# Kernel tuning notes

Hardware: AMD Instinct MI355X
Metric: run time of the kernel (lower is better)

The kernel has to match this reference:

```python
import jax, jax.numpy as jnp
import numpy as np

B, F, H = 16384, 2048, 4096   # batch, n_features, n_hidden
D, K = 4096, 2048             # num_of_demos, num_of_features


def setup_inputs() -> dict:
    key = jax.random.key(0)
    ks = jax.random.split(key, 16)
    s = 0.02
    return {
        "x": jax.random.normal(ks[0], (B, F), jnp.float32),
        "demo_metric": jax.random.uniform(ks[1], (D, K), jnp.float32),
        "alpha": jax.random.normal(ks[2], (K,), jnp.float32),
        "sample_loss": jax.random.uniform(ks[3], (D, K), jnp.float32),
        "subdom_constant": jax.random.uniform(ks[4], (1,), jnp.float32),
        "num_of_demos": D,
        "num_of_features": K,
        "W1": jax.random.normal(ks[5], (F, H), jnp.float32) * s,
        "b1": jnp.zeros((H,), jnp.float32),
        "W2": jax.random.normal(ks[6], (H, H), jnp.float32) * s,
        "b2": jnp.zeros((H,), jnp.float32),
        "W3": jax.random.normal(ks[7], (H, H), jnp.float32) * s,
        "b3": jnp.zeros((H,), jnp.float32),
        "W4": jax.random.normal(ks[8], (H, 2), jnp.float32) * s,
        "b4": jnp.zeros((2,), jnp.float32),
    }


def reference(x, demo_metric, alpha, sample_loss, subdom_constant,
              num_of_demos, num_of_features,
              W1, b1, W2, b2, W3, b3, W4, b4):
    # subdom hinge loss: max(alpha_k * (sample_loss_jk - demo_loss_jk) + 1, 0) - c
    margin = alpha[None, :] * (sample_loss - demo_metric) + 1.0  # [D, K]
    subdom = jnp.maximum(margin, 0.0) - subdom_constant          # broadcast c
    loss = jnp.sum(subdom)

    # MLP classifier (dropout = identity at inference) + sigmoid
    h = jax.nn.relu(x @ W1 + b1)
    h = jax.nn.relu(h @ W2 + b2)
    h = jax.nn.relu(h @ W3 + b3)
    probs = jax.nn.sigmoid(h @ W4 + b4)  # [B, 2]
    return (loss, probs)
```

## Files before the change

### kernel.cpp

```cpp
#include <hip/hip_runtime.h>
#include <cstdint>
#include <cstddef>

typedef unsigned short u16;
typedef __attribute__((ext_vector_type(8))) __bf16 bf16x8;
typedef __attribute__((ext_vector_type(4))) float f32x4;

__device__ __forceinline__ u16 f2bf(float f) {
  union { float f; unsigned u; } v; v.f = f;
  unsigned r = v.u + 0x7FFFu + ((v.u >> 16) & 1u);
  return (u16)(r >> 16);
}
__device__ __forceinline__ float bf2f(unsigned h) {
  union { unsigned u; float f; } v; v.u = h << 16;
  return v.f;
}

__global__ void init_loss_kernel(const float* __restrict__ c,
                                 const int* __restrict__ D,
                                 const int* __restrict__ K,
                                 float* __restrict__ out) {
  out[0] = -c[0] * (float)D[0] * (float)K[0];
}

__global__ void subdom_kernel(const float4* __restrict__ dm,
                              const float4* __restrict__ sl,
                              const float4* __restrict__ alpha4,
                              float* __restrict__ out, int n4, int k4mask) {
  const int stride = gridDim.x * blockDim.x;
  float s = 0.f;
  for (int i = blockIdx.x * blockDim.x + threadIdx.x; i < n4; i += stride) {
    float4 d = dm[i], l = sl[i], a = alpha4[i & k4mask];
    s += fmaxf(fmaf(a.x, l.x - d.x, 1.f), 0.f);
    s += fmaxf(fmaf(a.y, l.y - d.y, 1.f), 0.f);
    s += fmaxf(fmaf(a.z, l.z - d.z, 1.f), 0.f);
    s += fmaxf(fmaf(a.w, l.w - d.w, 1.f), 0.f);
  }
#pragma unroll
  for (int off = 32; off > 0; off >>= 1) s += __shfl_down(s, off, 64);
  __shared__ float red[4];
  const int lane = threadIdx.x & 63, wave = threadIdx.x >> 6;
  if (lane == 0) red[wave] = s;
  __syncthreads();
  if (threadIdx.x == 0) atomicAdd(out, red[0] + red[1] + red[2] + red[3]);
}

__global__ void cast_f32_bf16_kernel(const float4* __restrict__ in,
                                     u16* __restrict__ out, int n4) {
  const int stride = gridDim.x * blockDim.x;
  for (int i = blockIdx.x * blockDim.x + threadIdx.x; i < n4; i += stride) {
    float4 v = in[i];
    uint2 p;
    p.x = (unsigned)f2bf(v.x) | ((unsigned)f2bf(v.y) << 16);
    p.y = (unsigned)f2bf(v.z) | ((unsigned)f2bf(v.w) << 16);
    ((uint2*)out)[i] = p;
  }
}

__global__ void transpose_cast_kernel(const float* __restrict__ in,
                                      u16* __restrict__ out, int K, int N) {
  __shared__ float tile[32][33];
  const int bx = blockIdx.x * 32;
  const int by = blockIdx.y * 32;
  const int tx = threadIdx.x, ty = threadIdx.y;
#pragma unroll
  for (int i = ty; i < 32; i += 8)
    tile[i][tx] = in[(size_t)(by + i) * N + bx + tx];
  __syncthreads();
#pragma unroll
  for (int i = ty; i < 32; i += 8)
    out[(size_t)(bx + i) * K + by + tx] = f2bf(tile[tx][i]);
}


__device__ __forceinline__ void gload_lds16(const void* g, void* l) {
  __builtin_amdgcn_global_load_lds(
      (const __attribute__((address_space(1))) void*)g,
      (__attribute__((address_space(3))) void*)l, 16, 0, 0);
}

#define VMW(N) asm volatile("s_waitcnt vmcnt(" #N ")" ::: "memory")

#define STAGE_A(BU, KH, TK)                                                   \
  do {                                                                        \
    gload_lds16(A + aoff0 + (size_t)((TK) * 64 + (KH) * 32),                  \
                (void*)(As + ((BU)*2 + (KH)) * 8192 + wslot));                \
    gload_lds16(A + aoff1 + (size_t)((TK) * 64 + (KH) * 32),                  \
                (void*)(As + ((BU)*2 + (KH)) * 8192 + 4096 + wslot));         \
  } while (0)

#define STAGE_B(BU, KH, TK)                                                   \
  do {                                                                        \
    gload_lds16(Bt + boff0 + (size_t)((TK) * 64 + (KH) * 32),                 \
                (void*)(Bs + ((BU)*2 + (KH)) * 8192 + wslot));                \
    gload_lds16(Bt + boff1 + (size_t)((TK) * 64 + (KH) * 32),                 \
                (void*)(Bs + ((BU)*2 + (KH)) * 8192 + 4096 + wslot));         \
  } while (0)

#define PH(BU, KH, MH, LB, STAGE_CODE, WAIT_CODE)                             \
  {                                                                           \
    const u16* Ar_ = As + ((BU)*2 + (KH)) * 8192 + (MH)*2048 + aread;         \
    bf16x8 af_[4];                                                            \
    af_[0] = *(const bf16x8*)(Ar_);                                           \
    af_[1] = *(const bf16x8*)(Ar_ + 512);                                     \
    af_[2] = *(const bf16x8*)(Ar_ + 1024);                                    \
    af_[3] = *(const bf16x8*)(Ar_ + 1536);                                    \
    if (LB) {                                                                 \
      const u16* Br_ = Bs + ((BU)*2 + (KH)) * 8192 + bread;                   \
      bfr[0] = *(const bf16x8*)(Br_);                                         \
      bfr[1] = *(const bf16x8*)(Br_ + 512);                                   \
      bfr[2] = *(const bf16x8*)(Br_ + 1024);                                  \
      bfr[3] = *(const bf16x8*)(Br_ + 1536);                                  \
    }                                                                         \
    STAGE_CODE;                                                               \
    __builtin_amdgcn_s_barrier();                                             \
    __builtin_amdgcn_s_setprio(1);                                            \
    _Pragma("unroll") for (int f_ = 0; f_ < 4; ++f_)                          \
      _Pragma("unroll") for (int n_ = 0; n_ < 4; ++n_)                        \
        acc[(MH)*4 + f_][n_] = __builtin_amdgcn_mfma_f32_16x16x32_bf16(       \
            af_[f_], bfr[n_], acc[(MH)*4 + f_][n_], 0, 0, 0);                 \
    __builtin_amdgcn_s_setprio(0);                                            \
    WAIT_CODE;                                                                \
    __builtin_amdgcn_s_barrier();                                             \
  }

__global__ __launch_bounds__(512, 2) void gemm256(
    const u16* __restrict__ A, const u16* __restrict__ Bt,
    const float* __restrict__ bias, u16* __restrict__ C,
    int M, int N, int K, int act) {
  __shared__ __align__(16) u16 As[4 * 8192];
  __shared__ __align__(16) u16 Bs[4 * 8192];

  const int gx = gridDim.x;
  const int bid = blockIdx.x + blockIdx.y * gx;
  const int cpx = (gx * gridDim.y) >> 3;
  const int tilei = (bid & 7) * cpx + (bid >> 3);
  const int m0 = (tilei / gx) * 256;
  const int n0 = (tilei % gx) * 256;

  const int tid = threadIdx.x;
  const int wave = tid >> 6, lane = tid & 63;
  const int l15 = lane & 15, quad = lane >> 4;
  const int wm = wave >> 2, wn = wave & 3;

  const int sl8 = ((quad ^ (l15 & 3)) << 3);
  const int aread = (wm * 128 + l15) * 32 + sl8;
  const int bread = (wn * 64 + l15) * 32 + sl8;
  const int wslot = wave * 512;

  const int r0 = tid >> 2;
  const int kn = (((tid & 3) ^ (r0 & 3)) << 3);
  const size_t aoff0 = (size_t)(m0 + r0) * K + kn;
  const size_t aoff1 = aoff0 + (size_t)128 * K;
  const size_t boff0 = (size_t)(n0 + r0) * K + kn;
  const size_t boff1 = boff0 + (size_t)128 * K;

  f32x4 acc[8][4];
#pragma unroll
  for (int i = 0; i < 8; ++i)
#pragma unroll
    for (int j = 0; j < 4; ++j) acc[i][j] = (f32x4){0.f, 0.f, 0.f, 0.f};
  bf16x8 bfr[4];

  STAGE_A(0, 0, 0); STAGE_B(0, 0, 0);
  STAGE_A(0, 1, 0); STAGE_B(0, 1, 0);
  STAGE_A(1, 0, 1); STAGE_B(1, 0, 1);
  VMW(8);
  __builtin_amdgcn_s_barrier();

  const int niter = K >> 7;
  for (int it = 0; it < niter; ++it) {
    const int t1 = 2 * it + 1;
    const bool nl = (it + 1 < niter);
    PH(0, 0, 0, 1, { STAGE_A(1, 1, t1); }, {});
    PH(0, 0, 1, 0, { STAGE_B(1, 1, t1); }, { VMW(8); });
    PH(0, 1, 0, 1, { if (nl) STAGE_A(0, 0, t1 + 1); }, {});
    PH(0, 1, 1, 0, { if (nl) STAGE_B(0, 0, t1 + 1); },
       { if (nl) { VMW(8); } else { VMW(4); } });
    PH(1, 0, 0, 1, { if (nl) STAGE_A(0, 1, t1 + 1); }, {});
    PH(1, 0, 1, 0, { if (nl) STAGE_B(0, 1, t1 + 1); },
       { if (nl) { VMW(8); } else { VMW(0); } });
    PH(1, 1, 0, 1, { if (nl) STAGE_A(1, 0, t1 + 2); }, {});
    PH(1, 1, 1, 0, { if (nl) STAGE_B(1, 0, t1 + 2); },
       { if (nl) { VMW(8); } });
  }

#pragma unroll
  for (int mi = 0; mi < 8; ++mi) {
    const int row = m0 + wm * 128 + (mi >> 2) * 64 + (mi & 3) * 16 + quad * 4;
#pragma unroll
    for (int j = 0; j < 4; ++j) {
      const int col = n0 + wn * 64 + j * 16 + l15;
      const float bv = bias[col];
#pragma unroll
      for (int r = 0; r < 4; ++r) {
        float v = acc[mi][j][r] + bv;
        if (act) v = fmaxf(v, 0.f);
        C[(size_t)(row + r) * N + col] = f2bf(v);
      }
    }
  }
}

__global__ __launch_bounds__(256) void head_kernel(
    const u16* __restrict__ h, const float2* __restrict__ W4,
    const float* __restrict__ b4, float* __restrict__ out, int H) {
  const int row = blockIdx.x;
  const u16* hr = h + (size_t)row * H;
  const int tid = threadIdx.x;
  float p0 = 0.f, p1 = 0.f;
#pragma unroll
  for (int ii = 0; ii < 2; ++ii) {
    const int base = tid * 16 + ii * 8;
    const uint4 hv = *(const uint4*)(hr + base);
    const unsigned uu[4] = {hv.x, hv.y, hv.z, hv.w};
#pragma unroll
    for (int j = 0; j < 4; ++j) {
      float a0 = bf2f(uu[j] & 0xffffu);
      float a1 = bf2f(uu[j] >> 16);
      float2 w0 = W4[base + 2 * j];
      float2 w1 = W4[base + 2 * j + 1];
      p0 += a0 * w0.x + a1 * w1.x;
      p1 += a0 * w0.y + a1 * w1.y;
    }
  }
#pragma unroll
  for (int off = 32; off > 0; off >>= 1) {
    p0 += __shfl_down(p0, off, 64);
    p1 += __shfl_down(p1, off, 64);
  }
  __shared__ float r0[4], r1[4];
  const int lane = tid & 63, wave = tid >> 6;
  if (lane == 0) { r0[wave] = p0; r1[wave] = p1; }
  __syncthreads();
  if (tid == 0) {
    float l0 = r0[0] + r0[1] + r0[2] + r0[3] + b4[0];
    float l1 = r1[0] + r1[1] + r1[2] + r1[3] + b4[1];
    out[1 + row * 2] = 1.f / (1.f + __expf(-l0));
    out[2 + row * 2] = 1.f / (1.f + __expf(-l1));
  }
}

extern "C" void kernel_launch(void* const* d_in, const int* in_sizes, int n_in,
                              void* d_out, int out_size, void* d_ws,
                              size_t ws_size, hipStream_t stream) {
  (void)in_sizes; (void)n_in; (void)out_size; (void)ws_size;
  const float* x  = (const float*)d_in[0];
  const float* dm = (const float*)d_in[1];
  const float* al = (const float*)d_in[2];
  const float* sl = (const float*)d_in[3];
  const float* sc = (const float*)d_in[4];
  const int*   nd = (const int*)d_in[5];
  const int*   nf = (const int*)d_in[6];
  const float* W1 = (const float*)d_in[7];
  const float* b1 = (const float*)d_in[8];
  const float* W2 = (const float*)d_in[9];
  const float* b2 = (const float*)d_in[10];
  const float* W3 = (const float*)d_in[11];
  const float* b3 = (const float*)d_in[12];
  const float* W4 = (const float*)d_in[13];
  const float* b4 = (const float*)d_in[14];
  float* out = (float*)d_out;

  const int B = 16384, F = 2048, H = 4096, D = 4096, K = 2048;

  char* ws = (char*)d_ws;
  u16* xb = (u16*)ws;
  u16* wt = (u16*)(ws + (size_t)B * F * 2);
  u16* hA = (u16*)(ws + (size_t)B * F * 2 + (size_t)H * H * 2);
  u16* hB = hA + (size_t)B * H;

  init_loss_kernel<<<1, 1, 0, stream>>>(sc, nd, nf, out);
  subdom_kernel<<<1024, 256, 0, stream>>>((const float4*)dm, (const float4*)sl,
                                          (const float4*)al, out, D * K / 4,
                                          K / 4 - 1);
  cast_f32_bf16_kernel<<<4096, 256, 0, stream>>>((const float4*)x, xb, B * F / 4);
  transpose_cast_kernel<<<dim3(H / 32, F / 32), dim3(32, 8), 0, stream>>>(W1, wt, F, H);
  gemm256<<<dim3(H / 256, B / 256), 512, 0, stream>>>(xb, wt, b1, hA, B, H, F, 1);
  transpose_cast_kernel<<<dim3(H / 32, H / 32), dim3(32, 8), 0, stream>>>(W2, wt, H, H);
  gemm256<<<dim3(H / 256, B / 256), 512, 0, stream>>>(hA, wt, b2, hB, B, H, H, 1);
  transpose_cast_kernel<<<dim3(H / 32, H / 32), dim3(32, 8), 0, stream>>>(W3, wt, H, H);
  gemm256<<<dim3(H / 256, B / 256), 512, 0, stream>>>(hB, wt, b3, hA, B, H, H, 1);
  head_kernel<<<B, 256, 0, stream>>>(hA, (const float2*)W4, b4, out, H);
}
```

Baseline: 1.773 ms.

## Restructure GEMM LDS layout to 64-wide K chunks with new staging schedule

Reorganizes the bf16 GEMM's shared-memory tiles from two 32-wide K halves into full 64-wide K rows with an 8-way XOR swizzle. The 8-phase loop is re-split so each phase covers an M-half by N-half quadrant with two MFMAs along K. Global-to-LDS prefetch is rescheduled with new vmcnt wait counts. The aim is fewer LDS fragment reloads, wider contiguous global loads and better overlap of loads with MFMA. It adds risk from the intricate wait-count and buffer-reuse ordering.

```diff
diff --git a/kernel.cpp b/kernel.cpp
--- a/kernel.cpp
+++ b/kernel.cpp
@@ -80,45 +80,42 @@
 }
 
 #define VMW(N) asm volatile("s_waitcnt vmcnt(" #N ")" ::: "memory")
-
-#define STAGE_A(BU, KH, TK)                                                   \
-  do {                                                                        \
-    gload_lds16(A + aoff0 + (size_t)((TK) * 64 + (KH) * 32),                  \
-                (void*)(As + ((BU)*2 + (KH)) * 8192 + wslot));                \
-    gload_lds16(A + aoff1 + (size_t)((TK) * 64 + (KH) * 32),                  \
-                (void*)(As + ((BU)*2 + (KH)) * 8192 + 4096 + wslot));         \
-  } while (0)
-
-#define STAGE_B(BU, KH, TK)                                                   \
-  do {                                                                        \
-    gload_lds16(Bt + boff0 + (size_t)((TK) * 64 + (KH) * 32),                 \
-                (void*)(Bs + ((BU)*2 + (KH)) * 8192 + wslot));                \
-    gload_lds16(Bt + boff1 + (size_t)((TK) * 64 + (KH) * 32),                 \
-                (void*)(Bs + ((BU)*2 + (KH)) * 8192 + 4096 + wslot));         \
-  } while (0)
-
-#define PH(BU, KH, MH, LB, STAGE_CODE, WAIT_CODE)                             \
+#define MF(a, b, c) __builtin_amdgcn_mfma_f32_16x16x32_bf16(a, b, c, 0, 0, 0)
+
+#define STAGE_A(BU, Q, TK)                                                    \
+  gload_lds16(A + aGbase + (size_t)((Q)*64) * K + (size_t)(TK)*64,            \
+              (void*)(As + ((BU)*4 + (Q)) * 4096 + swave))
+
+#define STAGE_B(BU, NH, HH, TK)                                               \
+  gload_lds16(Bt + bGbase + (size_t)((NH)*32 + (HH)*128) * K +                \
+                  (size_t)(TK)*64,                                            \
+              (void*)(Bs + ((BU)*2 + (NH)) * 8192 + (HH)*4096 + swave))
+
+#define PHASE(BUF, MH, NH, LA, LB, BF, STAGE_CODE, WAIT_CODE)                 \
   {                                                                           \
-    const u16* Ar_ = As + ((BU)*2 + (KH)) * 8192 + (MH)*2048 + aread;         \
-    bf16x8 af_[4];                                                            \
-    af_[0] = *(const bf16x8*)(Ar_);                                           \
-    af_[1] = *(const bf16x8*)(Ar_ + 512);                                     \
-    af_[2] = *(const bf16x8*)(Ar_ + 1024);                                    \
-    af_[3] = *(const bf16x8*)(Ar_ + 1536);                                    \
+    if (LA) {                                                                 \
+      const u16* Ar_ = As + ((BUF)*4 + (wm << 1) + (MH)) * 4096 + abase;      \
+      _Pragma("unroll") for (int f_ = 0; f_ < 4; ++f_) {                      \
+        af0[f_] = *(const bf16x8*)(Ar_ + f_ * 1024 + aslot0);                 \
+        af1[f_] = *(const bf16x8*)(Ar_ + f_ * 1024 + aslot1);                 \
+      }                                                                       \
+    }                                                                         \
     if (LB) {                                                                 \
-      const u16* Br_ = Bs + ((BU)*2 + (KH)) * 8192 + bread;                   \
-      bfr[0] = *(const bf16x8*)(Br_);                                         \
-      bfr[1] = *(const bf16x8*)(Br_ + 512);                                   \
-      bfr[2] = *(const bf16x8*)(Br_ + 1024);                                  \
-      bfr[3] = *(const bf16x8*)(Br_ + 1536);                                  \
+      const u16* Br_ = Bs + ((BUF)*2 + (NH)) * 8192 + bbase;                  \
+      BF[0] = *(const bf16x8*)(Br_ + aslot0);                                 \
+      BF[1] = *(const bf16x8*)(Br_ + aslot1);                                 \
+      BF[2] = *(const bf16x8*)(Br_ + 1024 + aslot0);                          \
+      BF[3] = *(const bf16x8*)(Br_ + 1024 + aslot1);                          \
     }                                                                         \
     STAGE_CODE;                                                               \
     __builtin_amdgcn_s_barrier();                                             \
     __builtin_amdgcn_s_setprio(1);                                            \
-    _Pragma("unroll") for (int f_ = 0; f_ < 4; ++f_)                          \
-      _Pragma("unroll") for (int n_ = 0; n_ < 4; ++n_)                        \
-        acc[(MH)*4 + f_][n_] = __builtin_amdgcn_mfma_f32_16x16x32_bf16(       \
-            af_[f_], bfr[n_], acc[(MH)*4 + f_][n_], 0, 0, 0);                 \
+    _Pragma("unroll") for (int f_ = 0; f_ < 4; ++f_) {                        \
+      acc[(MH)*4 + f_][(NH)*2 + 0] = MF(af0[f_], BF[0], acc[(MH)*4 + f_][(NH)*2 + 0]); \
+      acc[(MH)*4 + f_][(NH)*2 + 0] = MF(af1[f_], BF[1], acc[(MH)*4 + f_][(NH)*2 + 0]); \
+      acc[(MH)*4 + f_][(NH)*2 + 1] = MF(af0[f_], BF[2], acc[(MH)*4 + f_][(NH)*2 + 1]); \
+      acc[(MH)*4 + f_][(NH)*2 + 1] = MF(af1[f_], BF[3], acc[(MH)*4 + f_][(NH)*2 + 1]); \
+    }                                                                         \
     __builtin_amdgcn_s_setprio(0);                                            \
     WAIT_CODE;                                                                \
     __builtin_amdgcn_s_barrier();                                             \
@@ -128,8 +125,8 @@
     const u16* __restrict__ A, const u16* __restrict__ Bt,
     const float* __restrict__ bias, u16* __restrict__ C,
     int M, int N, int K, int act) {
-  __shared__ __align__(16) u16 As[4 * 8192];
-  __shared__ __align__(16) u16 Bs[4 * 8192];
+  __shared__ __align__(16) u16 As[2 * 4 * 4096];
+  __shared__ __align__(16) u16 Bs[2 * 2 * 8192];
 
   const int gx = gridDim.x;
   const int bid = blockIdx.x + blockIdx.y * gx;
@@ -142,47 +139,58 @@
   const int wave = tid >> 6, lane = tid & 63;
   const int l15 = lane & 15, quad = lane >> 4;
   const int wm = wave >> 2, wn = wave & 3;
-
-  const int sl8 = ((quad ^ (l15 & 3)) << 3);
-  const int aread = (wm * 128 + l15) * 32 + sl8;
-  const int bread = (wn * 64 + l15) * 32 + sl8;
-  const int wslot = wave * 512;
-
-  const int r0 = tid >> 2;
-  const int kn = (((tid & 3) ^ (r0 & 3)) << 3);
-  const size_t aoff0 = (size_t)(m0 + r0) * K + kn;
-  const size_t aoff1 = aoff0 + (size_t)128 * K;
-  const size_t boff0 = (size_t)(n0 + r0) * K + kn;
-  const size_t boff1 = boff0 + (size_t)128 * K;
+  const int lsw = l15 & 7;
+
+  const int aslot0 = ((quad ^ lsw) << 3);
+  const int aslot1 = (((4 + quad) ^ lsw) << 3);
+  const int abase = l15 * 64;
+  const int bbase = (wn * 32 + l15) * 64;
+
+  const int srow = tid >> 3;
+  const int skch = ((tid & 7) ^ (srow & 7)) << 3;
+  const int brow = ((srow >> 5) << 6) + (srow & 31);
+  const size_t aGbase = (size_t)(m0 + srow) * K + skch;
+  const size_t bGbase = (size_t)(n0 + brow) * K + skch;
+  const int swave = wave * 512;
 
   f32x4 acc[8][4];
 #pragma unroll
   for (int i = 0; i < 8; ++i)
 #pragma unroll
     for (int j = 0; j < 4; ++j) acc[i][j] = (f32x4){0.f, 0.f, 0.f, 0.f};
-  bf16x8 bfr[4];
-
-  STAGE_A(0, 0, 0); STAGE_B(0, 0, 0);
-  STAGE_A(0, 1, 0); STAGE_B(0, 1, 0);
-  STAGE_A(1, 0, 1); STAGE_B(1, 0, 1);
-  VMW(8);
+  bf16x8 af0[4], af1[4], bfr0[4], bfr1[4];
+
+  STAGE_A(0, 0, 0); STAGE_A(0, 1, 0); STAGE_A(0, 2, 0); STAGE_A(0, 3, 0);
+  STAGE_B(0, 0, 0, 0); STAGE_B(0, 0, 1, 0);
+  STAGE_B(0, 1, 0, 0); STAGE_B(0, 1, 1, 0);
+  STAGE_A(1, 0, 1); STAGE_A(1, 2, 1);
+  VMW(2);
   __builtin_amdgcn_s_barrier();
 
   const int niter = K >> 7;
   for (int it = 0; it < niter; ++it) {
-    const int t1 = 2 * it + 1;
+    const int t1 = 2 * it + 1, t2 = 2 * it + 2, t3 = 2 * it + 3;
     const bool nl = (it + 1 < niter);
-    PH(0, 0, 0, 1, { STAGE_A(1, 1, t1); }, {});
-    PH(0, 0, 1, 0, { STAGE_B(1, 1, t1); }, { VMW(8); });
-    PH(0, 1, 0, 1, { if (nl) STAGE_A(0, 0, t1 + 1); }, {});
-    PH(0, 1, 1, 0, { if (nl) STAGE_B(0, 0, t1 + 1); },
-       { if (nl) { VMW(8); } else { VMW(4); } });
-    PH(1, 0, 0, 1, { if (nl) STAGE_A(0, 1, t1 + 1); }, {});
-    PH(1, 0, 1, 0, { if (nl) STAGE_B(0, 1, t1 + 1); },
-       { if (nl) { VMW(8); } else { VMW(0); } });
-    PH(1, 1, 0, 1, { if (nl) STAGE_A(1, 0, t1 + 2); }, {});
-    PH(1, 1, 1, 0, { if (nl) STAGE_B(1, 0, t1 + 2); },
-       { if (nl) { VMW(8); } });
+    PHASE(0, 0, 0, 1, 1, bfr0,
+          { STAGE_B(1, 0, 0, t1); STAGE_B(1, 0, 1, t1); }, { VMW(6); });
+    PHASE(0, 0, 1, 0, 1, bfr1,
+          { STAGE_B(1, 1, 0, t1); STAGE_B(1, 1, 1, t1); }, { VMW(4); });
+    PHASE(0, 1, 0, 1, 0, bfr0,
+          { if (nl) { STAGE_A(0, 0, t2); STAGE_A(0, 2, t2); } }, {});
+    PHASE(0, 1, 1, 0, 0, bfr1,
+          { STAGE_A(1, 1, t1); STAGE_A(1, 3, t1); },
+          { if (nl) { VMW(6); } else { VMW(4); } });
+    PHASE(1, 0, 0, 1, 1, bfr0,
+          { if (nl) { STAGE_B(0, 0, 0, t2); STAGE_B(0, 0, 1, t2); } },
+          { if (nl) { VMW(6); } else { VMW(2); } });
+    PHASE(1, 0, 1, 0, 1, bfr1,
+          { if (nl) { STAGE_B(0, 1, 0, t2); STAGE_B(0, 1, 1, t2); } },
+          { if (nl) { VMW(4); } else { VMW(0); } });
+    PHASE(1, 1, 0, 1, 0, bfr0,
+          { if (nl) { STAGE_A(1, 0, t3); STAGE_A(1, 2, t3); } }, {});
+    PHASE(1, 1, 1, 0, 0, bfr1,
+          { if (nl) { STAGE_A(0, 1, t2); STAGE_A(0, 3, t2); } },
+          { if (nl) { VMW(6); } });
   }
 
 #pragma unroll
```

Result: slower. 1.812 ms (+2.2%).
